# Optimization experiments

Hardware: AMD Instinct MI355X
Metric: run time of the kernel (lower is better)

The kernel has to match this reference:

```python
import jax, jax.numpy as jnp
import numpy as np

B, S, H, N, D = 2, 2048, 1024, 16, 64  # batch, seq, hidden, heads, head_size
PAD = -30000.0


def setup_inputs() -> dict:
    key = jax.random.key(0)
    kx, kqkv, kout, krpe = jax.random.split(key, 4)
    x = jax.random.normal(kx, (B, S, H), jnp.float32)
    qkv = jax.random.normal(kqkv, (H, 3, N, D), jnp.float32) * H ** (-0.5)
    out_w = jax.random.normal(kout, (N, D, H), jnp.float32) * (N * D) ** (-0.5)
    # rpe_bias is zero-init in torch; use small randn so the bias path is exercised
    rpe_bias = jax.random.normal(krpe, (N, S), jnp.float32) * 0.02
    return {"x": x, "qkv": qkv, "out_w": out_w, "rpe_bias": rpe_bias}


def reference(x, qkv, out_w, rpe_bias):
    # q, k, v: [B, N, S, D]
    q, k, v = jnp.einsum('bsx,xMnd->Mbnsd', x, qkv)
    s = x.shape[1]
    a = jnp.einsum('bnsd,bntd->bnst', q, k) * q.shape[-1] ** (-0.5)
    # cumulative relative-position bias: bias[n, i, j] = cumsum(rpe)[n, i-j] for i>=j,
    # PAD otherwise (exactly what to_tril produces on the row-broadcast cumsum).
    cum = jnp.cumsum(rpe_bias[:, :s], axis=-1)            # [N, S]
    rel = jnp.arange(s)[:, None] - jnp.arange(s)[None, :]  # [S, S], i - j
    bias = jnp.where(rel >= 0, cum[:, jnp.clip(rel, 0)], PAD)  # [N, S, S]
    a = jax.nn.softmax(a + bias, axis=-1)
    mix = jnp.einsum('bnst,bntd->bnsd', a, v)
    return jnp.einsum('bnsd,ndx->bsx', mix, out_w)
```

## Files before the change

kernel.cpp:

```cpp
#include <hip/hip_runtime.h>
#include <hip/hip_bf16.h>
#include <cstdint>
#include <cstddef>

#define B_   2
#define S_   2048
#define H_   1024
#define NH   16
#define DH   64
#define LOG2E 1.4426950408889634f
#define SCALE2 (0.125f * LOG2E)

typedef __hip_bfloat16 bf16;
typedef short bf16x8 __attribute__((ext_vector_type(8)));
typedef float f32x4 __attribute__((ext_vector_type(4)));

#define MFMA16(a, b, c) __builtin_amdgcn_mfma_f32_16x16x32_bf16((a), (b), (c), 0, 0, 0)

__device__ __forceinline__ void async16(const void* g, void* l) {
  __builtin_amdgcn_global_load_lds(
      (const __attribute__((address_space(1))) void*)g,
      (__attribute__((address_space(3))) void*)l,
      16, 0, 0);
}
__device__ __forceinline__ void async4(const void* g, void* l) {
  __builtin_amdgcn_global_load_lds(
      (const __attribute__((address_space(1))) void*)g,
      (__attribute__((address_space(3))) void*)l,
      4, 0, 0);
}

__device__ __forceinline__ short bf16bits(float v) {
  bf16 t = __float2bfloat16(v);
  return *reinterpret_cast<short*>(&t);
}

__device__ __forceinline__ void tr_body(const float* __restrict__ src,
                                        bf16* __restrict__ dst, int R, int C,
                                        int c0, int r0, bf16 (*tile)[33], int tid) {
  int tx = tid & 31, ty = tid >> 5;
  for (int i = 0; i < 32; i += 8)
    tile[ty + i][tx] = __float2bfloat16(src[(size_t)(r0 + ty + i) * C + c0 + tx]);
  __syncthreads();
  for (int i = 0; i < 32; i += 8)
    dst[(size_t)(c0 + ty + i) * R + r0 + tx] = tile[tx][ty + i];
}

__global__ __launch_bounds__(256)
void prep(const float* __restrict__ x, bf16* __restrict__ xb,
          const float* __restrict__ qkv, bf16* __restrict__ qkvT,
          const float* __restrict__ outw, bf16* __restrict__ outwT,
          const float* __restrict__ rpe, float* __restrict__ cum) {
  __shared__ char pm[2176] __attribute__((aligned(16)));
  const int L = blockIdx.x, tid = threadIdx.x;
  if (L < 4096) {
    int i = (L * 256 + tid) * 4;
    float4 v = *(const float4*)(x + i);
    bf16 o[4] = {__float2bfloat16(v.x), __float2bfloat16(v.y),
                 __float2bfloat16(v.z), __float2bfloat16(v.w)};
    *(uint64_t*)(xb + i) = *(const uint64_t*)o;
  } else if (L < 7168) {
    int t = L - 4096;
    int cx = t % 96, ry = t / 96;
    tr_body(qkv, qkvT, 1024, 3072, cx * 32, ry * 32, (bf16(*)[33])pm, tid);
  } else if (L < 8192) {
    int t = L - 7168;
    int cx = t & 31, ry = t >> 5;
    tr_body(outw, outwT, 1024, 1024, cx * 32, ry * 32, (bf16(*)[33])pm, tid);
  } else {
    float* ssum = (float*)pm;
    int n = L - 8192;
    float loc[8];
    float s = 0.f;
    int base = tid * 8;
#pragma unroll
    for (int u = 0; u < 8; ++u) {
      loc[u] = rpe[n * S_ + base + u];
      s += loc[u];
    }
    ssum[tid] = s;
    __syncthreads();
    float own = s;
    for (int off = 1; off < 256; off <<= 1) {
      float v = (tid >= off) ? ssum[tid - off] : 0.f;
      __syncthreads();
      ssum[tid] += v;
      __syncthreads();
    }
    float run = ssum[tid] - own;
#pragma unroll
    for (int u = 0; u < 8; ++u) {
      run += loc[u];
      cum[n * S_ + base + u] = run * LOG2E;
    }
  }
}

template <int MODE>
__global__ __launch_bounds__(256, MODE == 0 ? 3 : 2)
void gemm_bt(const bf16* __restrict__ A, const bf16* __restrict__ Bt,
             bf16* __restrict__ C0, bf16* __restrict__ C1, bf16* __restrict__ C2,
             float* __restrict__ F0) {
  constexpr int NT = (MODE == 0) ? 4 : 2;
  constexpr int NB = NT * 32;
  constexpr int BUFSZ = 8192 + NB * 64;
  __shared__ char smem[MODE == 0 ? 36864 : 24576] __attribute__((aligned(16)));
  const int tid = threadIdx.x, lane = tid & 63, w = tid >> 6;
  const int lr = lane & 15, lq = lane >> 4;
  const int m0 = blockIdx.y * 128, n0 = blockIdx.x * NB;
  const int wm = (w & 1) * 64, wn = (w >> 1) * (NT * 16);

  f32x4 acc[4][NT] = {};

  auto stage = [&](int buf, int k0) {
    char* dst = smem + buf * BUFSZ;
#pragma unroll
    for (int t = 0; t < 2; ++t) {
      int c = t * 256 + tid;
      int row = c >> 2, ch = c & 3;
      int k8 = (ch ^ ((row >> 1) & 3)) * 8;
      async16(A + (size_t)(m0 + row) * 1024 + k0 + k8, dst + c * 16);
    }
#pragma unroll
    for (int t = 0; t < NB / 64; ++t) {
      int c = t * 256 + tid;
      int row = c >> 2, ch = c & 3;
      int k8 = (ch ^ ((row >> 1) & 3)) * 8;
      async16(Bt + (size_t)(n0 + row) * 1024 + k0 + k8, dst + 8192 + c * 16);
    }
  };

  stage(0, 0);

  for (int s = 0; s < 32; ++s) {
    const int bsel = s & 1;
    __syncthreads();

    if (s + 1 < 32) stage(bsel ^ 1, (s + 1) * 32);

    const bf16* As = (const bf16*)(smem + bsel * BUFSZ);
    const bf16* Bs = (const bf16*)(smem + bsel * BUFSZ + 8192);
    bf16x8 af[4], bfr[NT];
#pragma unroll
    for (int mt = 0; mt < 4; ++mt) {
      int row = wm + mt * 16 + lr;
      af[mt] = *(const bf16x8*)(As + row * 32 + ((lq ^ ((row >> 1) & 3)) << 3));
    }
#pragma unroll
    for (int nt = 0; nt < NT; ++nt) {
      int row = wn + nt * 16 + lr;
      bfr[nt] = *(const bf16x8*)(Bs + row * 32 + ((lq ^ ((row >> 1) & 3)) << 3));
    }
#pragma unroll
    for (int mt = 0; mt < 4; ++mt)
#pragma unroll
      for (int nt = 0; nt < NT; ++nt)
        acc[mt][nt] = MFMA16(af[mt], bfr[nt], acc[mt][nt]);
  }

  if (MODE == 0) {
    __syncthreads();
    bf16* E = (bf16*)smem + w * (64 * 72);
    const int cbase = n0 + wn;
    const int mm = cbase >> 10, nn = (cbase >> 6) & 15;
    const int bb = (m0 + wm) >> 11;
    const int sbase = (m0 + wm) & 2047;
    if (mm < 2) {
#pragma unroll
      for (int mt = 0; mt < 4; ++mt)
#pragma unroll
        for (int nt = 0; nt < 4; ++nt)
#pragma unroll
          for (int r = 0; r < 4; ++r)
            E[(mt * 16 + lq * 4 + r) * 72 + nt * 16 + lr] =
                __float2bfloat16(acc[mt][nt][r]);
      bf16* dst = (mm == 0 ? C0 : C1) +
                  ((size_t)(bb * NH + nn) * S_ + sbase) * DH;
#pragma unroll
      for (int it = 0; it < 8; ++it) {
        int c = it * 64 + lane;
        int rw = c >> 3, c8 = c & 7;
        *(uint4*)(dst + (size_t)rw * DH + c8 * 8) =
            *(const uint4*)(E + rw * 72 + c8 * 8);
      }
    } else {
#pragma unroll
      for (int mt = 0; mt < 4; ++mt)
#pragma unroll
        for (int nt = 0; nt < 4; ++nt)
#pragma unroll
          for (int r = 0; r < 4; ++r)
            E[(nt * 16 + lr) * 72 + mt * 16 + lq * 4 + r] =
                __float2bfloat16(acc[mt][nt][r]);
      bf16* dst = C2 + (size_t)(bb * NH + nn) * DH * S_;
#pragma unroll
      for (int it = 0; it < 8; ++it) {
        int c = it * 64 + lane;
        int dr = c >> 3, c8 = c & 7;
        *(uint4*)(dst + (size_t)dr * S_ + sbase + c8 * 8) =
            *(const uint4*)(E + dr * 72 + c8 * 8);
      }
    }
  } else {
#pragma unroll
    for (int mt = 0; mt < 4; ++mt)
#pragma unroll
      for (int nt = 0; nt < NT; ++nt)
#pragma unroll
        for (int r = 0; r < 4; ++r) {
          int rM = m0 + wm + mt * 16 + lq * 4 + r;
          int cN = n0 + wn + nt * 16 + lr;
          F0[(size_t)rM * 1024 + cN] = acc[mt][nt][r];
        }
  }
}

__device__ __forceinline__ void fa_stage(const bf16* __restrict__ k,
                                         const bf16* __restrict__ vt,
                                         const float* __restrict__ cumn,
                                         char* smem, int bn, int i0, int jb,
                                         int buf, int tid) {
  char* dst = smem + buf * 32768;
  const char* ksrc = (const char*)(k + ((size_t)bn * S_ + jb) * DH);
#pragma unroll
  for (int t = 0; t < 4; ++t) {
    int c = t * 256 + tid;
    int row = c >> 3, ch = c & 7;
    int cs = ch ^ ((row & 3) | ((row >> 1) & 4));
    async16(ksrc + row * 128 + cs * 16, dst + c * 16);
  }
  const char* vsrc = (const char*)(vt + (size_t)bn * DH * S_);
#pragma unroll
  for (int t = 0; t < 4; ++t) {
    int c = t * 256 + tid;
    int row = c >> 4, ch = c & 15;
    int cs = ch ^ (row & 15);
    async16(vsrc + (size_t)row * (S_ * 2) + jb * 2 + cs * 16,
            dst + 16384 + c * 16);
  }
  if (tid < 194) {
    float* cdst = (float*)(smem + 65536) + buf * 800;
    int base = i0 - jb - 127 + tid;
#pragma unroll
    for (int p = 0; p < 4; ++p) {
      int src = base + p;
      src = src < 0 ? 0 : (src > S_ - 1 ? S_ - 1 : src);
      async4(cumn + src, cdst + p * 200 + tid);
    }
  }
}

__global__ __launch_bounds__(256, 2)
void fa_kernel(const bf16* __restrict__ q, const bf16* __restrict__ k,
               const bf16* __restrict__ vt, const float* __restrict__ cum,
               bf16* __restrict__ mix) {
  __shared__ char smem[72192] __attribute__((aligned(16)));
  float* combL = (float*)(smem + 71936);

  const int tid = threadIdx.x, lane = tid & 63, w = tid >> 6;
  const int lr = lane & 15, lq = lane >> 4;
  const int rg = w & 1, jh = w >> 1;

  const int L = blockIdx.x;
  const int xcd = L & 7, slot = L >> 3;
  const int bn = xcd + 8 * (slot & 3);
  const int pp = slot >> 2;
  const int n = bn & (NH - 1);
  const int b = bn >> 4;
  const float* cumn = cum + n * S_;

  const int T0 = 31 - pp;
  const int T1 = pp;
  const int nu0 = (T0 + 2) >> 1;

  bf16x8 ones;
#pragma unroll
  for (int u = 0; u < 8; ++u) ones[u] = (short)0x3F80;
  const f32x4 fz = {0.f, 0.f, 0.f, 0.f};

  const int kkey = (lr & 3) | (((lr >> 2) & 1) << 2);

  bf16x8 qf[2][2];
  f32x4 oacc[2][4];
  f32x4 lacc[2];

  fa_stage(k, vt, cumn, smem, bn, T0 * 64, 0, 0, tid);

  int ti = T0, jt = 0, i0 = T0 * 64, nu = nu0;

  for (int g = 0; g < 17; ++g) {
    const int bsel = g & 1;
    const char* kb = smem + bsel * 32768;
    const char* vb = kb + 16384;
    const float* cumB = (const float*)(smem + 65536) + bsel * 800;
    const int jb = jt * 128;
    const bool diag = (jt == nu - 1);

    __syncthreads();

    if (g + 1 < 17) {
      int gn = g + 1, tin, jtn;
      if (gn < nu0) { tin = T0; jtn = gn; }
      else          { tin = T1; jtn = gn - nu0; }
      fa_stage(k, vt, cumn, smem, bn, tin * 64, jtn * 128, bsel ^ 1, tid);
    }

    if (jt == 0) {
      const bf16* qbase = q + ((size_t)bn * S_ + i0 + rg * 32) * DH;
#pragma unroll
      for (int is = 0; is < 2; ++is) {
#pragma unroll
        for (int kd = 0; kd < 2; ++kd)
          qf[is][kd] = *(const bf16x8*)(qbase + (is * 16 + lr) * DH + kd * 32 + lq * 8);
        lacc[is] = fz;
#pragma unroll
        for (int dt = 0; dt < 4; ++dt) oacc[is][dt] = fz;
      }
    }

    f32x4 sa[2][4] = {};
#pragma unroll
    for (int kd = 0; kd < 2; ++kd)
#pragma unroll
      for (int mm = 0; mm < 4; ++mm) {
        int kt = mm >> 1, nt2 = mm & 1;
        int krow = jh * 64 + kt * 32 + ((lr >> 2) << 3) + nt2 * 4 + (lr & 3);
        bf16x8 kf = *(const bf16x8*)(kb + krow * 128 +
                        (((kd * 4 + lq) ^ kkey) << 4));
        sa[0][mm] = MFMA16(kf, qf[0][kd], sa[0][mm]);
        sa[1][mm] = MFMA16(kf, qf[1][kd], sa[1][mm]);
      }

    const int doff = i0 - jb;
    bf16x8 pf[2][2];
#pragma unroll
    for (int is = 0; is < 2; ++is) {
      const int ilocI = rg * 32 + is * 16 + lr;
#pragma unroll
      for (int mm = 0; mm < 4; ++mm) {
        int kt = mm >> 1, nt2 = mm & 1;
        int jl = jh * 64 + kt * 32 + lq * 8 + nt2 * 4;
        int Xm3 = 124 + ilocI - jl;
        int ph = Xm3 & 3, b0 = Xm3 & ~3;
        f32x4 cv = *(const f32x4*)(cumB + ph * 200 + b0);
        if (!diag) {
#pragma unroll
          for (int r = 0; r < 4; ++r)
            pf[is][kt][nt2 * 4 + r] =
                bf16bits(exp2f(sa[is][mm][r] * SCALE2 + cv[3 - r]));
        } else {
#pragma unroll
          for (int r = 0; r < 4; ++r) {
            float pv = (doff + ilocI - jl - r >= 0)
                           ? exp2f(sa[is][mm][r] * SCALE2 + cv[3 - r])
                           : 0.f;
            pf[is][kt][nt2 * 4 + r] = bf16bits(pv);
          }
        }
      }
    }

#pragma unroll
    for (int kt = 0; kt < 2; ++kt) {
      lacc[0] = MFMA16(pf[0][kt], ones, lacc[0]);
      lacc[1] = MFMA16(pf[1][kt], ones, lacc[1]);
#pragma unroll
      for (int dt = 0; dt < 4; ++dt) {
        int vrow = dt * 16 + lr;
        bf16x8 vf = *(const bf16x8*)(vb + vrow * 256 +
                        (((jh * 8 + kt * 4 + lq) ^ (vrow & 15)) << 4));
        oacc[0][dt] = MFMA16(pf[0][kt], vf, oacc[0][dt]);
        oacc[1][dt] = MFMA16(pf[1][kt], vf, oacc[1][dt]);
      }
    }

    if (diag) {
      __syncthreads();
      float* scr = (float*)(smem + bsel * 32768) + rg * 2048;
      if (jh == 1) {
#pragma unroll
        for (int is = 0; is < 2; ++is) {
#pragma unroll
          for (int dt = 0; dt < 4; ++dt)
#pragma unroll
            for (int r = 0; r < 4; ++r) {
              int row = is * 16 + lq * 4 + r;
              int col = ((dt ^ lq) << 4) + lr;
              scr[row * 64 + col] = oacc[is][dt][r];
            }
          if (lr == 0)
#pragma unroll
            for (int r = 0; r < 4; ++r)
              combL[rg * 32 + is * 16 + lq * 4 + r] = lacc[is][r];
        }
      }
      __syncthreads();
      if (jh == 0) {
#pragma unroll
        for (int is = 0; is < 2; ++is) {
#pragma unroll
          for (int r = 0; r < 4; ++r)
            lacc[is][r] += combL[rg * 32 + is * 16 + lq * 4 + r];
#pragma unroll
          for (int dt = 0; dt < 4; ++dt)
#pragma unroll
            for (int r = 0; r < 4; ++r) {
              int row = is * 16 + lq * 4 + r;
              int col = ((dt ^ lq) << 4) + lr;
              oacc[is][dt][r] += scr[row * 64 + col];
            }
        }
#pragma unroll
        for (int is = 0; is < 2; ++is)
#pragma unroll
          for (int dt = 0; dt < 4; ++dt)
#pragma unroll
            for (int r = 0; r < 4; ++r) {
              int i = i0 + rg * 32 + is * 16 + lq * 4 + r;
              int d = dt * 16 + lr;
              mix[((size_t)(b * S_ + i) * NH + n) * DH + d] =
                  __float2bfloat16(oacc[is][dt][r] / lacc[is][r]);
            }
      }
      ti = T1; jt = 0; i0 = T1 * 64; nu = (T1 + 2) >> 1;
    } else {
      ++jt;
    }
  }
}

extern "C" void kernel_launch(void* const* d_in, const int* in_sizes, int n_in,
                              void* d_out, int out_size, void* d_ws, size_t ws_size,
                              hipStream_t stream) {
  const float* x     = (const float*)d_in[0];
  const float* qkv   = (const float*)d_in[1];
  const float* out_w = (const float*)d_in[2];
  const float* rpe   = (const float*)d_in[3];
  float* out = (float*)d_out;

  char* ws = (char*)d_ws;
  bf16* qkvT  = (bf16*)(ws + 0);
  bf16* outwT = (bf16*)(ws + 6291456);
  bf16* xb    = (bf16*)(ws + 8388608);
  bf16* qb    = (bf16*)(ws + 16777216);
  bf16* kb    = (bf16*)(ws + 25165824);
  bf16* vtb   = (bf16*)(ws + 33554432);
  bf16* mixb  = (bf16*)(ws + 41943040);
  float* cum  = (float*)(ws + 50331648);

  prep<<<8208, 256, 0, stream>>>(x, xb, qkv, qkvT, out_w, outwT, rpe, cum);
  gemm_bt<0><<<dim3(3072 / 128, 4096 / 128), 256, 0, stream>>>(xb, qkvT, qb, kb, vtb, nullptr);
  fa_kernel<<<512, 256, 0, stream>>>(qb, kb, vtb, cum, mixb);
  gemm_bt<1><<<dim3(1024 / 64, 4096 / 128), 256, 0, stream>>>(mixb, outwT, nullptr, nullptr, nullptr, out);
}
```

Measured before the change: 178.3 us.

## Split flash-attention keys across four waves and read padded cumsum bias from global

Each of the four waves in the attention block now owns all 64 query rows and a 32-key slice of the 128-key tile, instead of a 2x2 split over rows and keys. The per-tile async staging of the cumulative bias into LDS is dropped. The bias is now read with unaligned vector loads straight from a zero-padded global cumsum row that the prep kernel writes. This cuts LDS use and staging work and reuses each K/V fragment across four query sub-tiles, at the cost of more registers, uncoalesced global bias reads, and a longer three-stage cross-wave reduction at diagonal tiles.

```diff
diff --git a/kernel.cpp b/kernel.cpp
--- a/kernel.cpp
+++ b/kernel.cpp
@@ -10,10 +10,13 @@
 #define DH   64
 #define LOG2E 1.4426950408889634f
 #define SCALE2 (0.125f * LOG2E)
+#define CUMPAD 132
+#define CUMROW (CUMPAD + S_)
 
 typedef __hip_bfloat16 bf16;
 typedef short bf16x8 __attribute__((ext_vector_type(8)));
 typedef float f32x4 __attribute__((ext_vector_type(4)));
+typedef f32x4 __attribute__((aligned(4))) f32x4u;
 
 #define MFMA16(a, b, c) __builtin_amdgcn_mfma_f32_16x16x32_bf16((a), (b), (c), 0, 0, 0)
 
@@ -22,12 +25,6 @@
       (const __attribute__((address_space(1))) void*)g,
       (__attribute__((address_space(3))) void*)l,
       16, 0, 0);
-}
-__device__ __forceinline__ void async4(const void* g, void* l) {
-  __builtin_amdgcn_global_load_lds(
-      (const __attribute__((address_space(1))) void*)g,
-      (__attribute__((address_space(3))) void*)l,
-      4, 0, 0);
 }
 
 __device__ __forceinline__ short bf16bits(float v) {
@@ -70,6 +67,8 @@
   } else {
     float* ssum = (float*)pm;
     int n = L - 8192;
+    float* crow = cum + (size_t)n * CUMROW;
+    if (tid < CUMPAD) crow[tid] = 0.f;
     float loc[8];
     float s = 0.f;
     int base = tid * 8;
@@ -91,7 +90,7 @@
 #pragma unroll
     for (int u = 0; u < 8; ++u) {
       run += loc[u];
-      cum[n * S_ + base + u] = run * LOG2E;
+      crow[CUMPAD + base + u] = run * LOG2E;
     }
   }
 }
@@ -135,7 +134,6 @@
   for (int s = 0; s < 32; ++s) {
     const int bsel = s & 1;
     __syncthreads();
-
     if (s + 1 < 32) stage(bsel ^ 1, (s + 1) * 32);
 
     const bf16* As = (const bf16*)(smem + bsel * BUFSZ);
@@ -217,8 +215,7 @@
 
 __device__ __forceinline__ void fa_stage(const bf16* __restrict__ k,
                                          const bf16* __restrict__ vt,
-                                         const float* __restrict__ cumn,
-                                         char* smem, int bn, int i0, int jb,
+                                         char* smem, int bn, int jb,
                                          int buf, int tid) {
   char* dst = smem + buf * 32768;
   const char* ksrc = (const char*)(k + ((size_t)bn * S_ + jb) * DH);
@@ -238,28 +235,18 @@
     async16(vsrc + (size_t)row * (S_ * 2) + jb * 2 + cs * 16,
             dst + 16384 + c * 16);
   }
-  if (tid < 194) {
-    float* cdst = (float*)(smem + 65536) + buf * 800;
-    int base = i0 - jb - 127 + tid;
-#pragma unroll
-    for (int p = 0; p < 4; ++p) {
-      int src = base + p;
-      src = src < 0 ? 0 : (src > S_ - 1 ? S_ - 1 : src);
-      async4(cumn + src, cdst + p * 200 + tid);
-    }
-  }
 }
 
 __global__ __launch_bounds__(256, 2)
 void fa_kernel(const bf16* __restrict__ q, const bf16* __restrict__ k,
                const bf16* __restrict__ vt, const float* __restrict__ cum,
                bf16* __restrict__ mix) {
-  __shared__ char smem[72192] __attribute__((aligned(16)));
-  float* combL = (float*)(smem + 71936);
+  __shared__ char smem[66304] __attribute__((aligned(16)));
+  float* combL = (float*)(smem + 65536);
 
   const int tid = threadIdx.x, lane = tid & 63, w = tid >> 6;
   const int lr = lane & 15, lq = lane >> 4;
-  const int rg = w & 1, jh = w >> 1;
+  const int jh = w;
 
   const int L = blockIdx.x;
   const int xcd = L & 7, slot = L >> 3;
@@ -267,7 +254,7 @@
   const int pp = slot >> 2;
   const int n = bn & (NH - 1);
   const int b = bn >> 4;
-  const float* cumn = cum + n * S_;
+  const float* cumnP = cum + (size_t)n * CUMROW + CUMPAD;
 
   const int T0 = 31 - pp;
   const int T1 = pp;
@@ -280,35 +267,34 @@
 
   const int kkey = (lr & 3) | (((lr >> 2) & 1) << 2);
 
-  bf16x8 qf[2][2];
-  f32x4 oacc[2][4];
-  f32x4 lacc[2];
-
-  fa_stage(k, vt, cumn, smem, bn, T0 * 64, 0, 0, tid);
-
-  int ti = T0, jt = 0, i0 = T0 * 64, nu = nu0;
+  bf16x8 qf[4][2];
+  f32x4 oacc[4][4];
+  f32x4 lacc[4];
+
+  fa_stage(k, vt, smem, bn, 0, 0, tid);
+
+  int jt = 0, i0 = T0 * 64, nu = nu0;
 
   for (int g = 0; g < 17; ++g) {
     const int bsel = g & 1;
     const char* kb = smem + bsel * 32768;
     const char* vb = kb + 16384;
-    const float* cumB = (const float*)(smem + 65536) + bsel * 800;
     const int jb = jt * 128;
     const bool diag = (jt == nu - 1);
 
     __syncthreads();
 
     if (g + 1 < 17) {
-      int gn = g + 1, tin, jtn;
-      if (gn < nu0) { tin = T0; jtn = gn; }
-      else          { tin = T1; jtn = gn - nu0; }
-      fa_stage(k, vt, cumn, smem, bn, tin * 64, jtn * 128, bsel ^ 1, tid);
+      int gn = g + 1, jtn;
+      if (gn < nu0) jtn = gn;
+      else          jtn = gn - nu0;
+      fa_stage(k, vt, smem, bn, jtn * 128, bsel ^ 1, tid);
     }
 
     if (jt == 0) {
-      const bf16* qbase = q + ((size_t)bn * S_ + i0 + rg * 32) * DH;
-#pragma unroll
-      for (int is = 0; is < 2; ++is) {
+      const bf16* qbase = q + ((size_t)bn * S_ + i0) * DH;
+#pragma unroll
+      for (int is = 0; is < 4; ++is) {
 #pragma unroll
         for (int kd = 0; kd < 2; ++kd)
           qf[is][kd] = *(const bf16x8*)(qbase + (is * 16 + lr) * DH + kd * 32 + lq * 8);
@@ -318,111 +304,125 @@
       }
     }
 
-    f32x4 sa[2][4] = {};
+    f32x4 sa[4][2] = {};
 #pragma unroll
     for (int kd = 0; kd < 2; ++kd)
 #pragma unroll
-      for (int mm = 0; mm < 4; ++mm) {
-        int kt = mm >> 1, nt2 = mm & 1;
-        int krow = jh * 64 + kt * 32 + ((lr >> 2) << 3) + nt2 * 4 + (lr & 3);
+      for (int nt2 = 0; nt2 < 2; ++nt2) {
+        int krow = jh * 32 + ((lr >> 2) << 3) + nt2 * 4 + (lr & 3);
         bf16x8 kf = *(const bf16x8*)(kb + krow * 128 +
                         (((kd * 4 + lq) ^ kkey) << 4));
-        sa[0][mm] = MFMA16(kf, qf[0][kd], sa[0][mm]);
-        sa[1][mm] = MFMA16(kf, qf[1][kd], sa[1][mm]);
+#pragma unroll
+        for (int is = 0; is < 4; ++is)
+          sa[is][nt2] = MFMA16(kf, qf[is][kd], sa[is][nt2]);
       }
 
     const int doff = i0 - jb;
-    bf16x8 pf[2][2];
-#pragma unroll
-    for (int is = 0; is < 2; ++is) {
-      const int ilocI = rg * 32 + is * 16 + lr;
-#pragma unroll
-      for (int mm = 0; mm < 4; ++mm) {
-        int kt = mm >> 1, nt2 = mm & 1;
-        int jl = jh * 64 + kt * 32 + lq * 8 + nt2 * 4;
-        int Xm3 = 124 + ilocI - jl;
-        int ph = Xm3 & 3, b0 = Xm3 & ~3;
-        f32x4 cv = *(const f32x4*)(cumB + ph * 200 + b0);
+    bf16x8 pf[4];
+#pragma unroll
+    for (int is = 0; is < 4; ++is) {
+      const int ilocI = is * 16 + lr;
+#pragma unroll
+      for (int nt2 = 0; nt2 < 2; ++nt2) {
+        int jl = jh * 32 + lq * 8 + nt2 * 4;
+        int gidx = doff + ilocI - jl - 3;
+        f32x4 cv = *(const f32x4u*)(cumnP + gidx);
         if (!diag) {
 #pragma unroll
           for (int r = 0; r < 4; ++r)
-            pf[is][kt][nt2 * 4 + r] =
-                bf16bits(exp2f(sa[is][mm][r] * SCALE2 + cv[3 - r]));
+            pf[is][nt2 * 4 + r] =
+                bf16bits(exp2f(sa[is][nt2][r] * SCALE2 + cv[3 - r]));
         } else {
 #pragma unroll
           for (int r = 0; r < 4; ++r) {
             float pv = (doff + ilocI - jl - r >= 0)
-                           ? exp2f(sa[is][mm][r] * SCALE2 + cv[3 - r])
+                           ? exp2f(sa[is][nt2][r] * SCALE2 + cv[3 - r])
                            : 0.f;
-            pf[is][kt][nt2 * 4 + r] = bf16bits(pv);
+            pf[is][nt2 * 4 + r] = bf16bits(pv);
           }
         }
       }
     }
 
 #pragma unroll
-    for (int kt = 0; kt < 2; ++kt) {
-      lacc[0] = MFMA16(pf[0][kt], ones, lacc[0]);
-      lacc[1] = MFMA16(pf[1][kt], ones, lacc[1]);
-#pragma unroll
-      for (int dt = 0; dt < 4; ++dt) {
-        int vrow = dt * 16 + lr;
-        bf16x8 vf = *(const bf16x8*)(vb + vrow * 256 +
-                        (((jh * 8 + kt * 4 + lq) ^ (vrow & 15)) << 4));
-        oacc[0][dt] = MFMA16(pf[0][kt], vf, oacc[0][dt]);
-        oacc[1][dt] = MFMA16(pf[1][kt], vf, oacc[1][dt]);
-      }
+    for (int is = 0; is < 4; ++is)
+      lacc[is] = MFMA16(pf[is], ones, lacc[is]);
+#pragma unroll
+    for (int dt = 0; dt < 4; ++dt) {
+      int vrow = dt * 16 + lr;
+      bf16x8 vf = *(const bf16x8*)(vb + vrow * 256 +
+                      (((jh * 4 + lq) ^ (vrow & 15)) << 4));
+#pragma unroll
+      for (int is = 0; is < 4; ++is)
+        oacc[is][dt] = MFMA16(pf[is], vf, oacc[is][dt]);
     }
 
     if (diag) {
       __syncthreads();
-      float* scr = (float*)(smem + bsel * 32768) + rg * 2048;
-      if (jh == 1) {
-#pragma unroll
-        for (int is = 0; is < 2; ++is) {
+      f32x4* scrq = (f32x4*)(smem + bsel * 32768);
+      if (jh == 1 || jh == 3) {
+        f32x4* dst = scrq + (jh == 1 ? 0 : 1024);
+#pragma unroll
+        for (int is = 0; is < 4; ++is)
+#pragma unroll
+          for (int dt = 0; dt < 4; ++dt)
+            dst[(is * 4 + dt) * 64 + lane] = oacc[is][dt];
+      }
+      if (jh >= 1 && lr == 0) {
+#pragma unroll
+        for (int is = 0; is < 4; ++is)
+#pragma unroll
+          for (int r = 0; r < 4; ++r)
+            combL[(jh - 1) * 64 + is * 16 + lq * 4 + r] = lacc[is][r];
+      }
+      __syncthreads();
+      if (jh == 0) {
+#pragma unroll
+        for (int is = 0; is < 4; ++is)
+#pragma unroll
+          for (int dt = 0; dt < 4; ++dt)
+            oacc[is][dt] += scrq[(is * 4 + dt) * 64 + lane];
+      } else if (jh == 2) {
+#pragma unroll
+        for (int is = 0; is < 4; ++is)
+#pragma unroll
+          for (int dt = 0; dt < 4; ++dt)
+            oacc[is][dt] += scrq[1024 + (is * 4 + dt) * 64 + lane];
+      }
+      __syncthreads();
+      if (jh == 2) {
+#pragma unroll
+        for (int is = 0; is < 4; ++is)
+#pragma unroll
+          for (int dt = 0; dt < 4; ++dt)
+            scrq[(is * 4 + dt) * 64 + lane] = oacc[is][dt];
+      }
+      __syncthreads();
+      if (jh == 0) {
+#pragma unroll
+        for (int is = 0; is < 4; ++is) {
+#pragma unroll
+          for (int dt = 0; dt < 4; ++dt)
+            oacc[is][dt] += scrq[(is * 4 + dt) * 64 + lane];
+#pragma unroll
+          for (int r = 0; r < 4; ++r)
+            lacc[is][r] += combL[is * 16 + lq * 4 + r] +
+                           combL[64 + is * 16 + lq * 4 + r] +
+                           combL[128 + is * 16 + lq * 4 + r];
+        }
+#pragma unroll
+        for (int is = 0; is < 4; ++is)
 #pragma unroll
           for (int dt = 0; dt < 4; ++dt)
 #pragma unroll
             for (int r = 0; r < 4; ++r) {
-              int row = is * 16 + lq * 4 + r;
-              int col = ((dt ^ lq) << 4) + lr;
-              scr[row * 64 + col] = oacc[is][dt][r];
-            }
-          if (lr == 0)
-#pragma unroll
-            for (int r = 0; r < 4; ++r)
-              combL[rg * 32 + is * 16 + lq * 4 + r] = lacc[is][r];
-        }
-      }
-      __syncthreads();
-      if (jh == 0) {
-#pragma unroll
-        for (int is = 0; is < 2; ++is) {
-#pragma unroll
-          for (int r = 0; r < 4; ++r)
-            lacc[is][r] += combL[rg * 32 + is * 16 + lq * 4 + r];
-#pragma unroll
-          for (int dt = 0; dt < 4; ++dt)
-#pragma unroll
-            for (int r = 0; r < 4; ++r) {
-              int row = is * 16 + lq * 4 + r;
-              int col = ((dt ^ lq) << 4) + lr;
-              oacc[is][dt][r] += scr[row * 64 + col];
-            }
-        }
-#pragma unroll
-        for (int is = 0; is < 2; ++is)
-#pragma unroll
-          for (int dt = 0; dt < 4; ++dt)
-#pragma unroll
-            for (int r = 0; r < 4; ++r) {
-              int i = i0 + rg * 32 + is * 16 + lq * 4 + r;
+              int i = i0 + is * 16 + lq * 4 + r;
               int d = dt * 16 + lr;
               mix[((size_t)(b * S_ + i) * NH + n) * DH + d] =
                   __float2bfloat16(oacc[is][dt][r] / lacc[is][r]);
             }
       }
-      ti = T1; jt = 0; i0 = T1 * 64; nu = (T1 + 2) >> 1;
+      jt = 0; i0 = T1 * 64; nu = (T1 + 2) >> 1;
     } else {
       ++jt;
     }
```

New measurement: 189.2 us. 1.06x slower.

## Split flash-attention key block across four waves per row group with 512-thread blocks

Applied to the files above, without the earlier changes.

The attention kernel moves from 256 to 512 threads per block, so each 128-key tile is split four ways across waves instead of two. This halves the score and PV work per wave and raises the number of waves resident per CU. The diagonal-tile combine becomes a two-level tree reduction through LDS with extra barriers, and the partial row sums from three waves are added. The cumulative-bias buffer gets a zero-padded prefix per head, and the staging loops are retuned for the larger thread count. The cost is more synchronisation, extra LDS traffic in the combine, and a register budget tightened by the launch bound of 512 threads with 4 blocks.

```diff
diff --git a/kernel.cpp b/kernel.cpp
--- a/kernel.cpp
+++ b/kernel.cpp
@@ -10,6 +10,8 @@
 #define DH   64
 #define LOG2E 1.4426950408889634f
 #define SCALE2 (0.125f * LOG2E)
+#define CUMPAD 132
+#define CUMROW (CUMPAD + S_)
 
 typedef __hip_bfloat16 bf16;
 typedef short bf16x8 __attribute__((ext_vector_type(8)));
@@ -70,6 +72,8 @@
   } else {
     float* ssum = (float*)pm;
     int n = L - 8192;
+    float* crow = cum + (size_t)n * CUMROW;
+    if (tid < CUMPAD) crow[tid] = 0.f;
     float loc[8];
     float s = 0.f;
     int base = tid * 8;
@@ -91,7 +95,7 @@
 #pragma unroll
     for (int u = 0; u < 8; ++u) {
       run += loc[u];
-      cum[n * S_ + base + u] = run * LOG2E;
+      crow[CUMPAD + base + u] = run * LOG2E;
     }
   }
 }
@@ -135,7 +139,6 @@
   for (int s = 0; s < 32; ++s) {
     const int bsel = s & 1;
     __syncthreads();
-
     if (s + 1 < 32) stage(bsel ^ 1, (s + 1) * 32);
 
     const bf16* As = (const bf16*)(smem + bsel * BUFSZ);
@@ -223,16 +226,16 @@
   char* dst = smem + buf * 32768;
   const char* ksrc = (const char*)(k + ((size_t)bn * S_ + jb) * DH);
 #pragma unroll
-  for (int t = 0; t < 4; ++t) {
-    int c = t * 256 + tid;
+  for (int t = 0; t < 2; ++t) {
+    int c = t * 512 + tid;
     int row = c >> 3, ch = c & 7;
     int cs = ch ^ ((row & 3) | ((row >> 1) & 4));
     async16(ksrc + row * 128 + cs * 16, dst + c * 16);
   }
   const char* vsrc = (const char*)(vt + (size_t)bn * DH * S_);
 #pragma unroll
-  for (int t = 0; t < 4; ++t) {
-    int c = t * 256 + tid;
+  for (int t = 0; t < 2; ++t) {
+    int c = t * 512 + tid;
     int row = c >> 4, ch = c & 15;
     int cs = ch ^ (row & 15);
     async16(vsrc + (size_t)row * (S_ * 2) + jb * 2 + cs * 16,
@@ -250,16 +253,16 @@
   }
 }
 
-__global__ __launch_bounds__(256, 2)
+__global__ __launch_bounds__(512, 4)
 void fa_kernel(const bf16* __restrict__ q, const bf16* __restrict__ k,
                const bf16* __restrict__ vt, const float* __restrict__ cum,
                bf16* __restrict__ mix) {
-  __shared__ char smem[72192] __attribute__((aligned(16)));
+  __shared__ char smem[72704] __attribute__((aligned(16)));
   float* combL = (float*)(smem + 71936);
 
   const int tid = threadIdx.x, lane = tid & 63, w = tid >> 6;
   const int lr = lane & 15, lq = lane >> 4;
-  const int rg = w & 1, jh = w >> 1;
+  const int jh = w & 3, rg = w >> 2;
 
   const int L = blockIdx.x;
   const int xcd = L & 7, slot = L >> 3;
@@ -267,7 +270,7 @@
   const int pp = slot >> 2;
   const int n = bn & (NH - 1);
   const int b = bn >> 4;
-  const float* cumn = cum + n * S_;
+  const float* cumn = cum + (size_t)n * CUMROW + CUMPAD;
 
   const int T0 = 31 - pp;
   const int T1 = pp;
@@ -286,7 +289,7 @@
 
   fa_stage(k, vt, cumn, smem, bn, T0 * 64, 0, 0, tid);
 
-  int ti = T0, jt = 0, i0 = T0 * 64, nu = nu0;
+  int jt = 0, i0 = T0 * 64, nu = nu0;
 
   for (int g = 0; g < 17; ++g) {
     const int bsel = g & 1;
@@ -295,6 +298,7 @@
     const float* cumB = (const float*)(smem + 65536) + bsel * 800;
     const int jb = jt * 128;
     const bool diag = (jt == nu - 1);
+    const int doff = i0 - jb;
 
     __syncthreads();
 
@@ -318,97 +322,108 @@
       }
     }
 
-    f32x4 sa[2][4] = {};
+    f32x4 sa[2][2] = {};
 #pragma unroll
     for (int kd = 0; kd < 2; ++kd)
 #pragma unroll
-      for (int mm = 0; mm < 4; ++mm) {
-        int kt = mm >> 1, nt2 = mm & 1;
-        int krow = jh * 64 + kt * 32 + ((lr >> 2) << 3) + nt2 * 4 + (lr & 3);
+      for (int nt2 = 0; nt2 < 2; ++nt2) {
+        int krow = jh * 32 + ((lr >> 2) << 3) + nt2 * 4 + (lr & 3);
         bf16x8 kf = *(const bf16x8*)(kb + krow * 128 +
                         (((kd * 4 + lq) ^ kkey) << 4));
-        sa[0][mm] = MFMA16(kf, qf[0][kd], sa[0][mm]);
-        sa[1][mm] = MFMA16(kf, qf[1][kd], sa[1][mm]);
-      }
-
-    const int doff = i0 - jb;
-    bf16x8 pf[2][2];
+        sa[0][nt2] = MFMA16(kf, qf[0][kd], sa[0][nt2]);
+        sa[1][nt2] = MFMA16(kf, qf[1][kd], sa[1][nt2]);
+      }
+
+    bf16x8 pf[2];
 #pragma unroll
     for (int is = 0; is < 2; ++is) {
       const int ilocI = rg * 32 + is * 16 + lr;
 #pragma unroll
-      for (int mm = 0; mm < 4; ++mm) {
-        int kt = mm >> 1, nt2 = mm & 1;
-        int jl = jh * 64 + kt * 32 + lq * 8 + nt2 * 4;
+      for (int nt2 = 0; nt2 < 2; ++nt2) {
+        int jl = jh * 32 + lq * 8 + nt2 * 4;
         int Xm3 = 124 + ilocI - jl;
         int ph = Xm3 & 3, b0 = Xm3 & ~3;
         f32x4 cv = *(const f32x4*)(cumB + ph * 200 + b0);
         if (!diag) {
 #pragma unroll
           for (int r = 0; r < 4; ++r)
-            pf[is][kt][nt2 * 4 + r] =
-                bf16bits(exp2f(sa[is][mm][r] * SCALE2 + cv[3 - r]));
+            pf[is][nt2 * 4 + r] =
+                bf16bits(exp2f(sa[is][nt2][r] * SCALE2 + cv[3 - r]));
         } else {
 #pragma unroll
           for (int r = 0; r < 4; ++r) {
             float pv = (doff + ilocI - jl - r >= 0)
-                           ? exp2f(sa[is][mm][r] * SCALE2 + cv[3 - r])
+                           ? exp2f(sa[is][nt2][r] * SCALE2 + cv[3 - r])
                            : 0.f;
-            pf[is][kt][nt2 * 4 + r] = bf16bits(pv);
+            pf[is][nt2 * 4 + r] = bf16bits(pv);
           }
         }
       }
     }
 
-#pragma unroll
-    for (int kt = 0; kt < 2; ++kt) {
-      lacc[0] = MFMA16(pf[0][kt], ones, lacc[0]);
-      lacc[1] = MFMA16(pf[1][kt], ones, lacc[1]);
-#pragma unroll
-      for (int dt = 0; dt < 4; ++dt) {
-        int vrow = dt * 16 + lr;
-        bf16x8 vf = *(const bf16x8*)(vb + vrow * 256 +
-                        (((jh * 8 + kt * 4 + lq) ^ (vrow & 15)) << 4));
-        oacc[0][dt] = MFMA16(pf[0][kt], vf, oacc[0][dt]);
-        oacc[1][dt] = MFMA16(pf[1][kt], vf, oacc[1][dt]);
-      }
+    lacc[0] = MFMA16(pf[0], ones, lacc[0]);
+    lacc[1] = MFMA16(pf[1], ones, lacc[1]);
+#pragma unroll
+    for (int dt = 0; dt < 4; ++dt) {
+      int vrow = dt * 16 + lr;
+      bf16x8 vf = *(const bf16x8*)(vb + vrow * 256 +
+                      (((jh * 4 + lq) ^ (vrow & 15)) << 4));
+      oacc[0][dt] = MFMA16(pf[0], vf, oacc[0][dt]);
+      oacc[1][dt] = MFMA16(pf[1], vf, oacc[1][dt]);
     }
 
     if (diag) {
       __syncthreads();
-      float* scr = (float*)(smem + bsel * 32768) + rg * 2048;
-      if (jh == 1) {
+      f32x4* scrq = (f32x4*)(smem + bsel * 32768) + rg * 1024;
+      if (jh == 1 || jh == 3) {
+        f32x4* dst = scrq + (jh == 1 ? 0 : 512);
+#pragma unroll
+        for (int is = 0; is < 2; ++is)
+#pragma unroll
+          for (int dt = 0; dt < 4; ++dt)
+            dst[(is * 4 + dt) * 64 + lane] = oacc[is][dt];
+      }
+      if (jh >= 1 && lr == 0) {
+#pragma unroll
+        for (int is = 0; is < 2; ++is)
+#pragma unroll
+          for (int r = 0; r < 4; ++r)
+            combL[(rg * 3 + jh - 1) * 32 + is * 16 + lq * 4 + r] = lacc[is][r];
+      }
+      __syncthreads();
+      if (jh == 0) {
+#pragma unroll
+        for (int is = 0; is < 2; ++is)
+#pragma unroll
+          for (int dt = 0; dt < 4; ++dt)
+            oacc[is][dt] += scrq[(is * 4 + dt) * 64 + lane];
+      } else if (jh == 2) {
+#pragma unroll
+        for (int is = 0; is < 2; ++is)
+#pragma unroll
+          for (int dt = 0; dt < 4; ++dt)
+            oacc[is][dt] += scrq[512 + (is * 4 + dt) * 64 + lane];
+      }
+      __syncthreads();
+      if (jh == 2) {
+#pragma unroll
+        for (int is = 0; is < 2; ++is)
+#pragma unroll
+          for (int dt = 0; dt < 4; ++dt)
+            scrq[(is * 4 + dt) * 64 + lane] = oacc[is][dt];
+      }
+      __syncthreads();
+      if (jh == 0) {
 #pragma unroll
         for (int is = 0; is < 2; ++is) {
 #pragma unroll
           for (int dt = 0; dt < 4; ++dt)
-#pragma unroll
-            for (int r = 0; r < 4; ++r) {
-              int row = is * 16 + lq * 4 + r;
-              int col = ((dt ^ lq) << 4) + lr;
-              scr[row * 64 + col] = oacc[is][dt][r];
-            }
-          if (lr == 0)
-#pragma unroll
-            for (int r = 0; r < 4; ++r)
-              combL[rg * 32 + is * 16 + lq * 4 + r] = lacc[is][r];
-        }
-      }
-      __syncthreads();
-      if (jh == 0) {
-#pragma unroll
-        for (int is = 0; is < 2; ++is) {
+            oacc[is][dt] += scrq[(is * 4 + dt) * 64 + lane];
 #pragma unroll
           for (int r = 0; r < 4; ++r)
-            lacc[is][r] += combL[rg * 32 + is * 16 + lq * 4 + r];
-#pragma unroll
-          for (int dt = 0; dt < 4; ++dt)
-#pragma unroll
-            for (int r = 0; r < 4; ++r) {
-              int row = is * 16 + lq * 4 + r;
-              int col = ((dt ^ lq) << 4) + lr;
-              oacc[is][dt][r] += scr[row * 64 + col];
-            }
+            lacc[is][r] += combL[(rg * 3 + 0) * 32 + is * 16 + lq * 4 + r] +
+                           combL[(rg * 3 + 1) * 32 + is * 16 + lq * 4 + r] +
+                           combL[(rg * 3 + 2) * 32 + is * 16 + lq * 4 + r];
         }
 #pragma unroll
         for (int is = 0; is < 2; ++is)
@@ -422,7 +437,7 @@
                   __float2bfloat16(oacc[is][dt][r] / lacc[is][r]);
             }
       }
-      ti = T1; jt = 0; i0 = T1 * 64; nu = (T1 + 2) >> 1;
+      jt = 0; i0 = T1 * 64; nu = (T1 + 2) >> 1;
     } else {
       ++jt;
     }
@@ -450,6 +465,6 @@
 
   prep<<<8208, 256, 0, stream>>>(x, xb, qkv, qkvT, out_w, outwT, rpe, cum);
   gemm_bt<0><<<dim3(3072 / 128, 4096 / 128), 256, 0, stream>>>(xb, qkvT, qb, kb, vtb, nullptr);
-  fa_kernel<<<512, 256, 0, stream>>>(qb, kb, vtb, cum, mixb);
+  fa_kernel<<<512, 512, 0, stream>>>(qb, kb, vtb, cum, mixb);
   gemm_bt<1><<<dim3(1024 / 64, 4096 / 128), 256, 0, stream>>>(mixb, outwT, nullptr, nullptr, nullptr, out);
 }
```

New measurement: 182.5 us. +2.4%, slower.

## Halve flash-attention tiles to 32 queries by 64 keys and double grid

Applied to the files above, without the earlier changes.

The attention kernel now processes 32-row query tiles against 64-key blocks instead of 64x128. Each wave holds one 16-row slice, and the grid doubles to 1024 blocks. Shared memory per block halves, which allows more resident blocks and finer causal load balance, at the cost of less K/V reuse per load and more loop iterations and barriers. The cumulative bias rows are also zero-padded at the front so negative indices no longer need a lower clamp.

```diff
diff --git a/kernel.cpp b/kernel.cpp
--- a/kernel.cpp
+++ b/kernel.cpp
@@ -10,6 +10,8 @@
 #define DH   64
 #define LOG2E 1.4426950408889634f
 #define SCALE2 (0.125f * LOG2E)
+#define CUMPAD 132
+#define CUMROW (CUMPAD + S_)
 
 typedef __hip_bfloat16 bf16;
 typedef short bf16x8 __attribute__((ext_vector_type(8)));
@@ -70,6 +72,8 @@
   } else {
     float* ssum = (float*)pm;
     int n = L - 8192;
+    float* crow = cum + (size_t)n * CUMROW;
+    if (tid < CUMPAD) crow[tid] = 0.f;
     float loc[8];
     float s = 0.f;
     int base = tid * 8;
@@ -91,7 +95,7 @@
 #pragma unroll
     for (int u = 0; u < 8; ++u) {
       run += loc[u];
-      cum[n * S_ + base + u] = run * LOG2E;
+      crow[CUMPAD + base + u] = run * LOG2E;
     }
   }
 }
@@ -135,7 +139,6 @@
   for (int s = 0; s < 32; ++s) {
     const int bsel = s & 1;
     __syncthreads();
-
     if (s + 1 < 32) stage(bsel ^ 1, (s + 1) * 32);
 
     const bf16* As = (const bf16*)(smem + bsel * BUFSZ);
@@ -220,10 +223,10 @@
                                          const float* __restrict__ cumn,
                                          char* smem, int bn, int i0, int jb,
                                          int buf, int tid) {
-  char* dst = smem + buf * 32768;
+  char* dst = smem + buf * 16384;
   const char* ksrc = (const char*)(k + ((size_t)bn * S_ + jb) * DH);
 #pragma unroll
-  for (int t = 0; t < 4; ++t) {
+  for (int t = 0; t < 2; ++t) {
     int c = t * 256 + tid;
     int row = c >> 3, ch = c & 7;
     int cs = ch ^ ((row & 3) | ((row >> 1) & 4));
@@ -231,21 +234,21 @@
   }
   const char* vsrc = (const char*)(vt + (size_t)bn * DH * S_);
 #pragma unroll
-  for (int t = 0; t < 4; ++t) {
+  for (int t = 0; t < 2; ++t) {
     int c = t * 256 + tid;
-    int row = c >> 4, ch = c & 15;
-    int cs = ch ^ (row & 15);
+    int row = c >> 3, ch = c & 7;
+    int cs = ch ^ (row & 7);
     async16(vsrc + (size_t)row * (S_ * 2) + jb * 2 + cs * 16,
-            dst + 16384 + c * 16);
-  }
-  if (tid < 194) {
-    float* cdst = (float*)(smem + 65536) + buf * 800;
-    int base = i0 - jb - 127 + tid;
-#pragma unroll
-    for (int p = 0; p < 4; ++p) {
-      int src = base + p;
-      src = src < 0 ? 0 : (src > S_ - 1 ? S_ - 1 : src);
-      async4(cumn + src, cdst + p * 200 + tid);
+            dst + 8192 + c * 16);
+  }
+  if (tid < 96) {
+    float* cdst = (float*)(smem + 32768) + buf * 416;
+    int base = i0 - jb - 63 + tid;
+#pragma unroll
+    for (int ph = 0; ph < 4; ++ph) {
+      int src = base + ph;
+      src = src > S_ - 1 ? S_ - 1 : src;
+      async4(cumn + src, cdst + ph * 104 + tid);
     }
   }
 }
@@ -254,23 +257,23 @@
 void fa_kernel(const bf16* __restrict__ q, const bf16* __restrict__ k,
                const bf16* __restrict__ vt, const float* __restrict__ cum,
                bf16* __restrict__ mix) {
-  __shared__ char smem[72192] __attribute__((aligned(16)));
-  float* combL = (float*)(smem + 71936);
+  __shared__ char smem[36224] __attribute__((aligned(16)));
+  float* combL = (float*)(smem + 36096);
 
   const int tid = threadIdx.x, lane = tid & 63, w = tid >> 6;
   const int lr = lane & 15, lq = lane >> 4;
-  const int rg = w & 1, jh = w >> 1;
+  const int jh = w & 1, rg = w >> 1;
 
   const int L = blockIdx.x;
   const int xcd = L & 7, slot = L >> 3;
   const int bn = xcd + 8 * (slot & 3);
-  const int pp = slot >> 2;
+  const int p = slot >> 2;
   const int n = bn & (NH - 1);
   const int b = bn >> 4;
-  const float* cumn = cum + n * S_;
-
-  const int T0 = 31 - pp;
-  const int T1 = pp;
+  const float* cumn = cum + (size_t)n * CUMROW + CUMPAD;
+
+  const int T0 = 63 - p;
+  const int T1 = p;
   const int nu0 = (T0 + 2) >> 1;
 
   bf16x8 ones;
@@ -280,149 +283,116 @@
 
   const int kkey = (lr & 3) | (((lr >> 2) & 1) << 2);
 
-  bf16x8 qf[2][2];
-  f32x4 oacc[2][4];
-  f32x4 lacc[2];
-
-  fa_stage(k, vt, cumn, smem, bn, T0 * 64, 0, 0, tid);
-
-  int ti = T0, jt = 0, i0 = T0 * 64, nu = nu0;
-
-  for (int g = 0; g < 17; ++g) {
+  bf16x8 qf[2];
+  f32x4 oacc[4];
+  f32x4 lacc;
+
+  fa_stage(k, vt, cumn, smem, bn, T0 * 32, 0, 0, tid);
+
+  int jt = 0, i0 = T0 * 32, nu = nu0;
+
+  for (int g = 0; g < 33; ++g) {
     const int bsel = g & 1;
-    const char* kb = smem + bsel * 32768;
-    const char* vb = kb + 16384;
-    const float* cumB = (const float*)(smem + 65536) + bsel * 800;
-    const int jb = jt * 128;
+    const char* kb = smem + bsel * 16384;
+    const char* vb = kb + 8192;
+    const float* cumB = (const float*)(smem + 32768) + bsel * 416;
+    const int jb = jt * 64;
     const bool diag = (jt == nu - 1);
+    const int doff = i0 - jb;
 
     __syncthreads();
 
-    if (g + 1 < 17) {
+    if (g + 1 < 33) {
       int gn = g + 1, tin, jtn;
       if (gn < nu0) { tin = T0; jtn = gn; }
       else          { tin = T1; jtn = gn - nu0; }
-      fa_stage(k, vt, cumn, smem, bn, tin * 64, jtn * 128, bsel ^ 1, tid);
+      fa_stage(k, vt, cumn, smem, bn, tin * 32, jtn * 64, bsel ^ 1, tid);
     }
 
     if (jt == 0) {
-      const bf16* qbase = q + ((size_t)bn * S_ + i0 + rg * 32) * DH;
-#pragma unroll
-      for (int is = 0; is < 2; ++is) {
-#pragma unroll
-        for (int kd = 0; kd < 2; ++kd)
-          qf[is][kd] = *(const bf16x8*)(qbase + (is * 16 + lr) * DH + kd * 32 + lq * 8);
-        lacc[is] = fz;
-#pragma unroll
-        for (int dt = 0; dt < 4; ++dt) oacc[is][dt] = fz;
-      }
-    }
-
-    f32x4 sa[2][4] = {};
+      const bf16* qbase = q + ((size_t)bn * S_ + i0 + rg * 16) * DH;
+#pragma unroll
+      for (int kd = 0; kd < 2; ++kd)
+        qf[kd] = *(const bf16x8*)(qbase + lr * DH + kd * 32 + lq * 8);
+      lacc = fz;
+#pragma unroll
+      for (int dt = 0; dt < 4; ++dt) oacc[dt] = fz;
+    }
+
+    f32x4 sa[2] = {};
 #pragma unroll
     for (int kd = 0; kd < 2; ++kd)
 #pragma unroll
-      for (int mm = 0; mm < 4; ++mm) {
-        int kt = mm >> 1, nt2 = mm & 1;
-        int krow = jh * 64 + kt * 32 + ((lr >> 2) << 3) + nt2 * 4 + (lr & 3);
+      for (int nt2 = 0; nt2 < 2; ++nt2) {
+        int krow = jh * 32 + ((lr >> 2) << 3) + nt2 * 4 + (lr & 3);
         bf16x8 kf = *(const bf16x8*)(kb + krow * 128 +
                         (((kd * 4 + lq) ^ kkey) << 4));
-        sa[0][mm] = MFMA16(kf, qf[0][kd], sa[0][mm]);
-        sa[1][mm] = MFMA16(kf, qf[1][kd], sa[1][mm]);
-      }
-
-    const int doff = i0 - jb;
-    bf16x8 pf[2][2];
-#pragma unroll
-    for (int is = 0; is < 2; ++is) {
-      const int ilocI = rg * 32 + is * 16 + lr;
-#pragma unroll
-      for (int mm = 0; mm < 4; ++mm) {
-        int kt = mm >> 1, nt2 = mm & 1;
-        int jl = jh * 64 + kt * 32 + lq * 8 + nt2 * 4;
-        int Xm3 = 124 + ilocI - jl;
-        int ph = Xm3 & 3, b0 = Xm3 & ~3;
-        f32x4 cv = *(const f32x4*)(cumB + ph * 200 + b0);
-        if (!diag) {
-#pragma unroll
-          for (int r = 0; r < 4; ++r)
-            pf[is][kt][nt2 * 4 + r] =
-                bf16bits(exp2f(sa[is][mm][r] * SCALE2 + cv[3 - r]));
-        } else {
-#pragma unroll
-          for (int r = 0; r < 4; ++r) {
-            float pv = (doff + ilocI - jl - r >= 0)
-                           ? exp2f(sa[is][mm][r] * SCALE2 + cv[3 - r])
-                           : 0.f;
-            pf[is][kt][nt2 * 4 + r] = bf16bits(pv);
-          }
+        sa[nt2] = MFMA16(kf, qf[kd], sa[nt2]);
+      }
+
+    const int iloc = rg * 16 + lr;
+    bf16x8 pf;
+#pragma unroll
+    for (int nt2 = 0; nt2 < 2; ++nt2) {
+      int jl = jh * 32 + lq * 8 + nt2 * 4;
+      int Xm3 = 60 + iloc - jl;
+      int ph = Xm3 & 3, b0 = Xm3 & ~3;
+      f32x4 cv = *(const f32x4*)(cumB + ph * 104 + b0);
+      if (!diag) {
+#pragma unroll
+        for (int r = 0; r < 4; ++r)
+          pf[nt2 * 4 + r] = bf16bits(exp2f(sa[nt2][r] * SCALE2 + cv[3 - r]));
+      } else {
+#pragma unroll
+        for (int r = 0; r < 4; ++r) {
+          float pv = (doff + iloc - jl - r >= 0)
+                         ? exp2f(sa[nt2][r] * SCALE2 + cv[3 - r])
+                         : 0.f;
+          pf[nt2 * 4 + r] = bf16bits(pv);
         }
       }
     }
 
-#pragma unroll
-    for (int kt = 0; kt < 2; ++kt) {
-      lacc[0] = MFMA16(pf[0][kt], ones, lacc[0]);
-      lacc[1] = MFMA16(pf[1][kt], ones, lacc[1]);
-#pragma unroll
-      for (int dt = 0; dt < 4; ++dt) {
-        int vrow = dt * 16 + lr;
-        bf16x8 vf = *(const bf16x8*)(vb + vrow * 256 +
-                        (((jh * 8 + kt * 4 + lq) ^ (vrow & 15)) << 4));
-        oacc[0][dt] = MFMA16(pf[0][kt], vf, oacc[0][dt]);
-        oacc[1][dt] = MFMA16(pf[1][kt], vf, oacc[1][dt]);
-      }
+    lacc = MFMA16(pf, ones, lacc);
+#pragma unroll
+    for (int dt = 0; dt < 4; ++dt) {
+      int vrow = dt * 16 + lr;
+      bf16x8 vf = *(const bf16x8*)(vb + vrow * 128 +
+                      (((jh * 4 + lq) ^ (vrow & 7)) << 4));
+      oacc[dt] = MFMA16(pf, vf, oacc[dt]);
     }
 
     if (diag) {
       __syncthreads();
-      float* scr = (float*)(smem + bsel * 32768) + rg * 2048;
+      f32x4* scrq = (f32x4*)(smem + bsel * 16384) + rg * 256;
       if (jh == 1) {
 #pragma unroll
-        for (int is = 0; is < 2; ++is) {
-#pragma unroll
-          for (int dt = 0; dt < 4; ++dt)
-#pragma unroll
-            for (int r = 0; r < 4; ++r) {
-              int row = is * 16 + lq * 4 + r;
-              int col = ((dt ^ lq) << 4) + lr;
-              scr[row * 64 + col] = oacc[is][dt][r];
-            }
-          if (lr == 0)
-#pragma unroll
-            for (int r = 0; r < 4; ++r)
-              combL[rg * 32 + is * 16 + lq * 4 + r] = lacc[is][r];
-        }
+        for (int dt = 0; dt < 4; ++dt)
+          scrq[dt * 64 + lane] = oacc[dt];
+        if (lr == 0)
+#pragma unroll
+          for (int r = 0; r < 4; ++r)
+            combL[rg * 16 + lq * 4 + r] = lacc[r];
       }
       __syncthreads();
       if (jh == 0) {
 #pragma unroll
-        for (int is = 0; is < 2; ++is) {
-#pragma unroll
-          for (int r = 0; r < 4; ++r)
-            lacc[is][r] += combL[rg * 32 + is * 16 + lq * 4 + r];
-#pragma unroll
-          for (int dt = 0; dt < 4; ++dt)
-#pragma unroll
-            for (int r = 0; r < 4; ++r) {
-              int row = is * 16 + lq * 4 + r;
-              int col = ((dt ^ lq) << 4) + lr;
-              oacc[is][dt][r] += scr[row * 64 + col];
-            }
-        }
-#pragma unroll
-        for (int is = 0; is < 2; ++is)
-#pragma unroll
-          for (int dt = 0; dt < 4; ++dt)
-#pragma unroll
-            for (int r = 0; r < 4; ++r) {
-              int i = i0 + rg * 32 + is * 16 + lq * 4 + r;
-              int d = dt * 16 + lr;
-              mix[((size_t)(b * S_ + i) * NH + n) * DH + d] =
-                  __float2bfloat16(oacc[is][dt][r] / lacc[is][r]);
-            }
-      }
-      ti = T1; jt = 0; i0 = T1 * 64; nu = (T1 + 2) >> 1;
+        for (int dt = 0; dt < 4; ++dt)
+          oacc[dt] += scrq[dt * 64 + lane];
+#pragma unroll
+        for (int r = 0; r < 4; ++r)
+          lacc[r] += combL[rg * 16 + lq * 4 + r];
+#pragma unroll
+        for (int dt = 0; dt < 4; ++dt)
+#pragma unroll
+          for (int r = 0; r < 4; ++r) {
+            int i = i0 + rg * 16 + lq * 4 + r;
+            int d = dt * 16 + lr;
+            mix[((size_t)(b * S_ + i) * NH + n) * DH + d] =
+                __float2bfloat16(oacc[dt][r] / lacc[r]);
+          }
+      }
+      jt = 0; i0 = T1 * 32; nu = (T1 + 2) >> 1;
     } else {
       ++jt;
     }
@@ -450,6 +420,6 @@
 
   prep<<<8208, 256, 0, stream>>>(x, xb, qkv, qkvT, out_w, outwT, rpe, cum);
   gemm_bt<0><<<dim3(3072 / 128, 4096 / 128), 256, 0, stream>>>(xb, qkvT, qb, kb, vtb, nullptr);
-  fa_kernel<<<512, 256, 0, stream>>>(qb, kb, vtb, cum, mixb);
+  fa_kernel<<<1024, 256, 0, stream>>>(qb, kb, vtb, cum, mixb);
   gemm_bt<1><<<dim3(1024 / 64, 4096 / 128), 256, 0, stream>>>(mixb, outwT, nullptr, nullptr, nullptr, out);
 }
```

After: 178.9 us. About the same (+0.4%).
